# Kernel optimization log

Hardware: AMD Instinct MI355X
Metric: run time of the kernel (lower is better)

The kernel has to match this reference:

```python
import jax, jax.numpy as jnp
import numpy as np

B, C, H, W = 8, 256, 128, 128
P = 7          # patch_size (odd)
N = 500        # n_infer (eval mode)
HIDDEN = C // 16  # reduction=16


def setup_inputs() -> dict:
    key = jax.random.key(0)
    ks = jax.random.split(key, 8)
    def s(k, shape, fan_in):
        return jax.random.normal(k, shape, jnp.float32) * (1.0 / np.sqrt(fan_in))
    return {
        "x_main": jax.random.normal(ks[0], (B, C, H, W), jnp.float32),
        "x_aux": jax.random.normal(ks[1], (B, C, H, W), jnp.float32),
        "scorer_w": s(ks[2], (C,), C),            # 1x1 conv C->1
        "scorer_b": s(ks[3], (1,), C),
        "fc1_w": s(ks[4], (3 * C, HIDDEN), 3 * C),
        "fc1_b": jnp.zeros((HIDDEN,), jnp.float32),
        "fc2_w": s(ks[5], (HIDDEN, C), HIDDEN),
        "fc2_b": jnp.zeros((C,), jnp.float32),
        "proj_w": s(ks[6], (C, C), C),
        "proj_b": jnp.zeros((C,), jnp.float32),
        "n": N,
    }


def _sample_patch_feats(feat, px, py):
    # feat: [C,H,W]; px,py: [n,p,p] pixel coords (align_corners=False convention).
    # Bilinear sample with zero padding, then pool 0.5*(mean+max) over the patch.
    c, h, w = feat.shape
    x0 = jnp.floor(px); y0 = jnp.floor(py)
    wx1 = px - x0; wy1 = py - y0
    def gather(yi, xi):
        valid = ((yi >= 0) & (yi < h) & (xi >= 0) & (xi < w)).astype(feat.dtype)
        yc = jnp.clip(yi, 0, h - 1).astype(jnp.int32)
        xc = jnp.clip(xi, 0, w - 1).astype(jnp.int32)
        return feat[:, yc, xc] * valid  # [C,n,p,p]
    patch = (gather(y0, x0) * ((1 - wy1) * (1 - wx1))
             + gather(y0, x0 + 1) * ((1 - wy1) * wx1)
             + gather(y0 + 1, x0) * (wy1 * (1 - wx1))
             + gather(y0 + 1, x0 + 1) * (wy1 * wx1))  # [C,n,p,p]
    v = 0.5 * (patch.mean(axis=(2, 3)) + patch.max(axis=(2, 3)))  # [C,n]
    return v.T  # [n,C]


def reference(x_main, x_aux, scorer_w, scorer_b, fc1_w, fc1_b, fc2_w, fc2_b, proj_w, proj_b, n):
    b, c, h, w = x_main.shape
    # saliency scores -> topk indices over flattened HW
    score = jax.nn.sigmoid(jnp.einsum('bchw,c->bhw', x_main, scorer_w) + scorer_b[0])
    score = score.reshape(b, h * w)
    _, idx = jax.lax.top_k(score, n)  # [b,n] int32
    idx_y = idx // w
    idx_x = idx - idx_y * w
    # build the (clamped) normalized grid exactly as the torch module does,
    # then convert to pixel coords: px = ((g+1)*W - 1)/2 (align_corners=False)
    r = P // 2
    d = jnp.arange(-r, r + 1, dtype=jnp.float32)
    yy, xx = jnp.meshgrid(d, d, indexing='ij')
    off_x = xx * (2.0 / w); off_y = yy * (2.0 / h)           # [p,p]
    cx = (idx_x.astype(jnp.float32) + 0.5) * (2.0 / w) - 1.0  # [b,n]
    cy = (idx_y.astype(jnp.float32) + 0.5) * (2.0 / h) - 1.0
    gx = jnp.clip(cx[:, :, None, None] + off_x, -1.0, 1.0)    # [b,n,p,p]
    gy = jnp.clip(cy[:, :, None, None] + off_y, -1.0, 1.0)
    px = ((gx + 1.0) * w - 1.0) * 0.5
    py = ((gy + 1.0) * h - 1.0) * 0.5
    sample = jax.vmap(_sample_patch_feats)
    v_main = sample(x_main, px, py)  # [b,n,C]
    v_aux = sample(x_aux, px, py)    # aux_in_proj is Identity (c_main==c_aux)
    # instance-level cross attention
    sim = jnp.einsum('bnc,bmc->bnm', v_main, v_aux) / jnp.sqrt(jnp.float32(c))
    attn = jax.nn.softmax(sim, axis=-1)
    v_hat = jnp.einsum('bnm,bmc->bnc', attn, v_aux)
    # gated fusion MLP
    z = jnp.concatenate([v_main, v_hat, v_main - v_hat], axis=-1)  # [b,n,3C]
    gate = jax.nn.sigmoid(jax.nn.relu(z @ fc1_w + fc1_b) @ fc2_w + fc2_b)
    v_fused = v_main + gate * (v_main - v_hat)
    v_inj = v_fused @ proj_w + proj_b  # [b,n,C]
    # scatter-add reinjection at the topk locations
    inject = jnp.zeros((b, h * w, c), x_main.dtype)
    inject = inject.at[jnp.arange(b)[:, None], idx].add(v_inj)
    inject = inject.reshape(b, h, w, c).transpose(0, 3, 1, 2)
    return x_main + inject
```

## Files before the change

### kernel.cpp

```cpp
#include <hip/hip_runtime.h>
#include <cstdint>
#include <cstddef>

#define HW    16384
#define CCH   256
#define WID   128
#define NB    8
#define NSEL  500
#define NPAD  512
#define CPG   16

__device__ __forceinline__ unsigned key_of(float f) {
  unsigned u = __float_as_uint(f);
  return (u & 0x80000000u) ? ~u : (u | 0x80000000u);
}

__global__ __launch_bounds__(256) void score_kernel(const float* __restrict__ x,
                                                    const float* __restrict__ w,
                                                    float* __restrict__ logits) {
  __shared__ float ws[CCH];
  int tid = threadIdx.x;
  ws[tid] = w[tid];
  __syncthreads();
  int pix = blockIdx.x * 256 + tid;
  int b = pix >> 14, p = pix & (HW - 1);
  const float* xp = x + ((size_t)b << 22) + p;
  float acc = 0.f;
#pragma unroll 16
  for (int c = 0; c < CCH; c++) acc += xp[(size_t)c * HW] * ws[c];
  logits[pix] = acc;
}

__global__ __launch_bounds__(1024) void topk_kernel(const float* __restrict__ logits,
                                                    int* __restrict__ idx_out,
                                                    int* __restrict__ map) {
  int b = blockIdx.x, tid = threadIdx.x;
  int lane = tid & 63, wave = tid >> 6;
  const float* lg = logits + (size_t)b * HW;
  __shared__ unsigned hist[256];
  __shared__ unsigned wtot[4];
  __shared__ unsigned wsum[16];
  __shared__ unsigned bc_prefix;
  __shared__ int bc_want;
  __shared__ int cnt;

  unsigned kreg[16];
#pragma unroll
  for (int j = 0; j < 4; j++) {
    float4 v = *(const float4*)&lg[tid * 16 + j * 4];
    kreg[4 * j + 0] = key_of(v.x);
    kreg[4 * j + 1] = key_of(v.y);
    kreg[4 * j + 2] = key_of(v.z);
    kreg[4 * j + 3] = key_of(v.w);
  }
  for (int p = tid; p < HW; p += 1024) map[(size_t)b * HW + p] = -1;

  unsigned prefix = 0;
  int want = NSEL;
  for (int shift = 24; shift >= 0; shift -= 8) {
    if (tid < 256) hist[tid] = 0;
    __syncthreads();
#pragma unroll
    for (int j = 0; j < 16; j++) {
      unsigned u = kreg[j];
      bool m = (shift == 24) || ((u >> (shift + 8)) == (prefix >> (shift + 8)));
      if (m) atomicAdd(&hist[(u >> shift) & 255u], 1u);
    }
    __syncthreads();
    unsigned h = (tid < 256) ? hist[tid] : 0u;
    unsigned v = h;
#pragma unroll
    for (int o = 1; o < 64; o <<= 1) {
      unsigned t = __shfl_down(v, o);
      if (lane < 64 - o) v += t;
    }
    if (tid < 256 && lane == 0) wtot[wave] = v;
    __syncthreads();
    if (tid < 256) {
      unsigned sfx = v;
      for (int w2 = wave + 1; w2 < 4; w2++) sfx += wtot[w2];
      unsigned above = sfx - h;
      if ((int)sfx >= want && (int)above < want) {
        bc_prefix = prefix | ((unsigned)tid << shift);
        bc_want = want - (int)above;
      }
    }
    __syncthreads();
    prefix = bc_prefix;
    want = bc_want;
  }
  unsigned thr = prefix;

  int local = 0;
#pragma unroll
  for (int j = 0; j < 16; j++) local += (kreg[j] == thr) ? 1 : 0;
  unsigned pv = (unsigned)local;
#pragma unroll
  for (int o = 1; o < 64; o <<= 1) {
    unsigned t = __shfl_up(pv, o);
    if (lane >= o) pv += t;
  }
  if (lane == 63) wsum[wave] = pv;
  if (tid == 0) cnt = 0;
  __syncthreads();
  unsigned woff = 0;
  for (int w2 = 0; w2 < wave; w2++) woff += wsum[w2];
  int rank = (int)(woff + pv) - local;
#pragma unroll
  for (int j = 0; j < 16; j++) {
    unsigned u = kreg[j];
    bool take = (u > thr);
    if (u == thr) { if (rank < want) take = true; rank++; }
    if (take) {
      int s = atomicAdd(&cnt, 1);
      int p = tid * 16 + j;
      idx_out[b * NPAD + s] = p;
      map[(size_t)b * HW + p] = s;
    }
  }
}

__device__ __forceinline__ void patch_weights(int p, int* xc, int* yc, float* wx, float* wy) {
  int iy = p >> 7, ix = p & (WID - 1);
#pragma unroll
  for (int d = 0; d < 7; d++) {
    int t = ix + d - 3;
    bool in = (t >= 0) && (t < WID);
    xc[d] = in ? t : (t < 0 ? 0 : WID - 1);
    wx[d] = in ? 1.f : 0.5f;
    t = iy + d - 3;
    in = (t >= 0) && (t < WID);
    yc[d] = in ? t : (t < 0 ? 0 : WID - 1);
    wy[d] = in ? 1.f : 0.5f;
  }
}

__global__ __launch_bounds__(512) void gather_dma_kernel(const float* __restrict__ xm,
                                                         const float* __restrict__ xa,
                                                         const int* __restrict__ idx,
                                                         float* __restrict__ vmainT,
                                                         float* __restrict__ vauxT) {
  extern __shared__ float plane2[];
  int g = blockIdx.x, b = blockIdx.y, z = blockIdx.z;
  int tid = threadIdx.x;
  int c0 = g * CPG;
  const float* src = (z == 0 ? xm : xa) + ((size_t)(b * CCH + c0)) * HW;
  float* dst = (z == 0 ? vmainT : vauxT) + (((size_t)(b * CCH + c0)) << 9);

  int t500 = (tid < NSEL) ? tid : 0;
  int p = idx[b * NPAD + t500];
  float wx[7], wy[7];
  int xc[7], yc[7], rb[7];
  patch_weights(p, xc, yc, wx, wy);
#pragma unroll
  for (int d = 0; d < 7; d++) rb[d] = yc[d] * WID;

#pragma unroll
  for (int j = 0; j < 8; j++) {
    int off = (tid + j * 512) * 4;
    __builtin_amdgcn_global_load_lds(
        (const __attribute__((address_space(1))) float*)(src + off),
        (__attribute__((address_space(3))) float*)(plane2 + off), 16, 0, 0);
  }
  __syncthreads();

  for (int c = 0; c < CPG; c++) {
    float* cur = plane2 + ((c & 1) ? HW : 0);
    float* nxt = plane2 + ((c & 1) ? 0 : HW);
    if (c + 1 < CPG) {
      const float* s2 = src + (size_t)(c + 1) * HW;
#pragma unroll
      for (int j = 0; j < 8; j++) {
        int off = (tid + j * 512) * 4;
        __builtin_amdgcn_global_load_lds(
            (const __attribute__((address_space(1))) float*)(s2 + off),
            (__attribute__((address_space(3))) float*)(nxt + off), 16, 0, 0);
      }
    }
    if (tid < NSEL) {
      float s = 0.f, mx = -INFINITY;
#pragma unroll
      for (int dy = 0; dy < 7; dy++) {
        float rs = 0.f, rm = -INFINITY;
        int rbb = rb[dy];
        float wyd = wy[dy];
#pragma unroll
        for (int dx = 0; dx < 7; dx++) {
          float v = cur[rbb + xc[dx]] * wx[dx];
          rs += v;
          rm = fmaxf(rm, v);
        }
        s += rs * wyd;
        mx = fmaxf(mx, rm * wyd);
      }
      dst[((size_t)c << 9) + tid] = 0.5f * (s * (1.f / 49.f) + mx);
    } else {
      dst[((size_t)c << 9) + tid] = 0.f;
    }
    __syncthreads();
  }
}

template <int M, int N, int K, bool AT, bool BT, bool BSHARED, int EPI>
__global__ __launch_bounds__(256) void gemm_kernel(const float* __restrict__ A,
                                                   const float* __restrict__ B,
                                                   float* __restrict__ C,
                                                   const float* __restrict__ bias) {
  constexpr int BM = 64, BN = 64, BK = 16;
  __shared__ float As[BK][BM + 4];
  __shared__ float Bs[BK][BN + 4];
  int tid = threadIdx.x;
  int bx = blockIdx.x, by = blockIdx.y, b = blockIdx.z;
  const float* Ab = A + (size_t)b * M * K;
  const float* Bb = BSHARED ? B : (B + (size_t)b * ((size_t)K * N));
  int tx = tid & 15, ty = tid >> 4;
  float acc[4][4] = {};

  for (int k0 = 0; k0 < K; k0 += BK) {
    if (!AT) {
      int ar = tid >> 2, ac4 = (tid & 3) * 4;
      const float4 av = *(const float4*)&Ab[(size_t)(by * BM + ar) * K + k0 + ac4];
      As[ac4 + 0][ar] = av.x; As[ac4 + 1][ar] = av.y;
      As[ac4 + 2][ar] = av.z; As[ac4 + 3][ar] = av.w;
    } else {
      int kr = tid >> 4, mc = (tid & 15) * 4;
      *(float4*)&As[kr][mc] = *(const float4*)&Ab[(size_t)(k0 + kr) * M + by * BM + mc];
    }
    if (!BT) {
      int br = tid >> 4, bc4 = (tid & 15) * 4;
      *(float4*)&Bs[br][bc4] = *(const float4*)&Bb[(size_t)(k0 + br) * N + bx * BN + bc4];
    } else {
      int nr = tid >> 2, kc4 = (tid & 3) * 4;
      const float4 bv = *(const float4*)&Bb[(size_t)(bx * BN + nr) * K + k0 + kc4];
      Bs[kc4 + 0][nr] = bv.x; Bs[kc4 + 1][nr] = bv.y;
      Bs[kc4 + 2][nr] = bv.z; Bs[kc4 + 3][nr] = bv.w;
    }
    __syncthreads();
#pragma unroll
    for (int kk = 0; kk < BK; kk++) {
      const float4 a = *(const float4*)&As[kk][ty * 4];
      const float4 bb = *(const float4*)&Bs[kk][tx * 4];
      float av[4] = {a.x, a.y, a.z, a.w};
      float bv[4] = {bb.x, bb.y, bb.z, bb.w};
#pragma unroll
      for (int rr = 0; rr < 4; rr++)
#pragma unroll
        for (int ss = 0; ss < 4; ss++) acc[rr][ss] += av[rr] * bv[ss];
    }
    __syncthreads();
  }
  if (EPI == 2) {
#pragma unroll
    for (int s = 0; s < 4; s++) {
      int col = bx * BN + tx * 4 + s;
      float bv = bias[col];
#pragma unroll
      for (int r = 0; r < 4; r++) {
        int row = by * BM + ty * 4 + r;
        C[((size_t)b * N + col) * M + row] = acc[r][s] + bv;
      }
    }
  } else {
    float scale = (EPI == 1) ? 0.0625f : 1.f;
#pragma unroll
    for (int r = 0; r < 4; r++) {
      int row = by * BM + ty * 4 + r;
#pragma unroll
      for (int s = 0; s < 4; s++) {
        int col = bx * BN + tx * 4 + s;
        C[((size_t)b * M + row) * N + col] = acc[r][s] * scale;
      }
    }
  }
}

__global__ __launch_bounds__(256) void softmax_kernel(float* __restrict__ sim) {
  int i = blockIdx.x, b = blockIdx.y, tid = threadIdx.x;
  float* row = sim + ((size_t)b * NPAD + i) * NPAD;
  float v0 = (tid < NSEL) ? row[tid] : -INFINITY;
  int j1 = tid + 256;
  float v1 = (j1 < NSEL) ? row[j1] : -INFINITY;
  float m = fmaxf(v0, v1);
  for (int o = 32; o; o >>= 1) m = fmaxf(m, __shfl_down(m, o));
  __shared__ float red[4];
  __shared__ float bm, bs;
  int wave = tid >> 6, lane = tid & 63;
  if (lane == 0) red[wave] = m;
  __syncthreads();
  if (tid == 0) bm = fmaxf(fmaxf(red[0], red[1]), fmaxf(red[2], red[3]));
  __syncthreads();
  m = bm;
  float e0 = (tid < NSEL) ? expf(v0 - m) : 0.f;
  float e1 = (j1 < NSEL) ? expf(v1 - m) : 0.f;
  float s = e0 + e1;
  for (int o = 32; o; o >>= 1) s += __shfl_down(s, o);
  if (lane == 0) red[wave] = s;
  __syncthreads();
  if (tid == 0) bs = 1.f / (red[0] + red[1] + red[2] + red[3]);
  __syncthreads();
  row[tid] = e0 * bs;
  row[j1] = e1 * bs;
}

__global__ __launch_bounds__(256) void mlp_kernel(const float* __restrict__ vmainT,
                                                  const float* __restrict__ vhat,
                                                  const float* __restrict__ fc1w,
                                                  const float* __restrict__ fc1b,
                                                  const float* __restrict__ fc2w,
                                                  const float* __restrict__ fc2b,
                                                  float* __restrict__ vfused) {
  int i = blockIdx.x, b = blockIdx.y, c = threadIdx.x;
  size_t base = ((size_t)b * NPAD + i) * CCH + c;
  float vm = vmainT[(((size_t)(b * CCH + c)) << 9) + i];
  float vh = vhat[base], vd = vm - vh;
  const float* w0 = fc1w + (size_t)c * 16;
  const float* w1 = fc1w + (size_t)(256 + c) * 16;
  const float* w2 = fc1w + (size_t)(512 + c) * 16;
  __shared__ float ph[256][17];
  __shared__ float part2[16][17];
  __shared__ float hsh[16];
#pragma unroll
  for (int k = 0; k < 16; k++) ph[c][k] = vm * w0[k] + vh * w1[k] + vd * w2[k];
  __syncthreads();
  int kk = c & 15, g = c >> 4;
  float part = 0.f;
#pragma unroll
  for (int j = 0; j < 16; j++) part += ph[g * 16 + j][kk];
  part2[g][kk] = part;
  __syncthreads();
  if (c < 16) {
    float s = fc1b[c];
#pragma unroll
    for (int g2 = 0; g2 < 16; g2++) s += part2[g2][c];
    hsh[c] = fmaxf(s, 0.f);
  }
  __syncthreads();
  float gte = fc2b[c];
#pragma unroll
  for (int k = 0; k < 16; k++) gte += hsh[k] * fc2w[k * 256 + c];
  gte = 1.f / (1.f + expf(-gte));
  vfused[base] = vm + gte * vd;
}

__global__ __launch_bounds__(256) void final_kernel(const float* __restrict__ x,
                                                    const int* __restrict__ map,
                                                    const float* __restrict__ vinjT,
                                                    float* __restrict__ out) {
  int gid = blockIdx.x * 256 + threadIdx.x;
  int p4 = gid & 4095;
  int c = (gid >> 12) & 255;
  int b = gid >> 20;
  size_t xoff = (((size_t)(b * 256 + c)) << 14) + ((size_t)p4 << 2);
  float4 xv = *(const float4*)(x + xoff);
  const int4 mv = *(const int4*)(map + ((size_t)b << 14) + (p4 << 2));
  const float* vt = vinjT + ((size_t)(b * 256 + c) << 9);
  if (mv.x >= 0) xv.x += vt[mv.x];
  if (mv.y >= 0) xv.y += vt[mv.y];
  if (mv.z >= 0) xv.z += vt[mv.z];
  if (mv.w >= 0) xv.w += vt[mv.w];
  *(float4*)(out + xoff) = xv;
}

extern "C" void kernel_launch(void* const* d_in, const int* in_sizes, int n_in,
                              void* d_out, int out_size, void* d_ws, size_t ws_size,
                              hipStream_t stream) {
  const float* x_main   = (const float*)d_in[0];
  const float* x_aux    = (const float*)d_in[1];
  const float* scorer_w = (const float*)d_in[2];
  const float* fc1_w = (const float*)d_in[4];
  const float* fc1_b = (const float*)d_in[5];
  const float* fc2_w = (const float*)d_in[6];
  const float* fc2_b = (const float*)d_in[7];
  const float* proj_w = (const float*)d_in[8];
  const float* proj_b = (const float*)d_in[9];
  (void)in_sizes; (void)n_in; (void)out_size; (void)ws_size;

  float* ws = (float*)d_ws;
  float* logits = ws;
  int*   idx    = (int*)(ws + 131072);
  int*   map    = (int*)(ws + 135168);
  float* vmainT = ws + 266240;
  float* vauxT  = ws + 1314816;
  float* vhat   = ws + 2363392;
  float* vfused = ws + 3411968;
  float* sim    = ws + 4460544;
  float* vinjT  = vhat;
  float* out = (float*)d_out;

  score_kernel<<<512, 256, 0, stream>>>(x_main, scorer_w, logits);
  topk_kernel<<<NB, 1024, 0, stream>>>(logits, idx, map);
  gather_dma_kernel<<<dim3(CCH / CPG, NB, 2), 512, 2 * HW * sizeof(float), stream>>>(
      x_main, x_aux, idx, vmainT, vauxT);
  gemm_kernel<NPAD, NPAD, CCH, true, false, false, 1>
      <<<dim3(8, 8, NB), 256, 0, stream>>>(vmainT, vauxT, sim, nullptr);
  softmax_kernel<<<dim3(NPAD, NB), 256, 0, stream>>>(sim);
  gemm_kernel<NPAD, CCH, NPAD, false, true, false, 0>
      <<<dim3(4, 8, NB), 256, 0, stream>>>(sim, vauxT, vhat, nullptr);
  mlp_kernel<<<dim3(NPAD, NB), 256, 0, stream>>>(vmainT, vhat, fc1_w, fc1_b,
                                                 fc2_w, fc2_b, vfused);
  gemm_kernel<NPAD, CCH, CCH, false, false, true, 2>
      <<<dim3(4, 8, NB), 256, 0, stream>>>(vfused, proj_w, vinjT, proj_b);
  final_kernel<<<32768, 256, 0, stream>>>(x_main, map, vinjT, out);
}
```

Measured before the change: 488.7 us.

## Fuse output copy into score pass and replace final pass with sparse scatter

The score kernel now writes x_main to the output with nontemporal stores while it reads it for the saliency dot product. That removes the final full-tensor read-and-write pass and the dense index map (its initialisation and lookups). Reinjection becomes a small scatter kernel that adds the projected vectors only at the top-k positions. The cost is an extra 128MB write inside the score kernel, which is a single pass with low parallelism (512 blocks), plus scattered read-modify-writes to the output.

```diff
diff --git a/kernel.cpp b/kernel.cpp
--- a/kernel.cpp
+++ b/kernel.cpp
@@ -15,9 +15,10 @@
   return (u & 0x80000000u) ? ~u : (u | 0x80000000u);
 }
 
-__global__ __launch_bounds__(256) void score_kernel(const float* __restrict__ x,
-                                                    const float* __restrict__ w,
-                                                    float* __restrict__ logits) {
+__global__ __launch_bounds__(256) void score_copy_kernel(const float* __restrict__ x,
+                                                         const float* __restrict__ w,
+                                                         float* __restrict__ logits,
+                                                         float* __restrict__ out) {
   __shared__ float ws[CCH];
   int tid = threadIdx.x;
   ws[tid] = w[tid];
@@ -25,15 +26,19 @@
   int pix = blockIdx.x * 256 + tid;
   int b = pix >> 14, p = pix & (HW - 1);
   const float* xp = x + ((size_t)b << 22) + p;
+  float* op = out + ((size_t)b << 22) + p;
   float acc = 0.f;
-#pragma unroll 16
-  for (int c = 0; c < CCH; c++) acc += xp[(size_t)c * HW] * ws[c];
+#pragma unroll 8
+  for (int c = 0; c < CCH; c++) {
+    float v = xp[(size_t)c * HW];
+    acc += v * ws[c];
+    __builtin_nontemporal_store(v, &op[(size_t)c * HW]);
+  }
   logits[pix] = acc;
 }
 
 __global__ __launch_bounds__(1024) void topk_kernel(const float* __restrict__ logits,
-                                                    int* __restrict__ idx_out,
-                                                    int* __restrict__ map) {
+                                                    int* __restrict__ idx_out) {
   int b = blockIdx.x, tid = threadIdx.x;
   int lane = tid & 63, wave = tid >> 6;
   const float* lg = logits + (size_t)b * HW;
@@ -53,7 +58,6 @@
     kreg[4 * j + 2] = key_of(v.z);
     kreg[4 * j + 3] = key_of(v.w);
   }
-  for (int p = tid; p < HW; p += 1024) map[(size_t)b * HW + p] = -1;
 
   unsigned prefix = 0;
   int want = NSEL;
@@ -113,9 +117,7 @@
     if (u == thr) { if (rank < want) take = true; rank++; }
     if (take) {
       int s = atomicAdd(&cnt, 1);
-      int p = tid * 16 + j;
-      idx_out[b * NPAD + s] = p;
-      map[(size_t)b * HW + p] = s;
+      idx_out[b * NPAD + s] = tid * 16 + j;
     }
   }
 }
@@ -342,23 +344,16 @@
   vfused[base] = vm + gte * vd;
 }
 
-__global__ __launch_bounds__(256) void final_kernel(const float* __restrict__ x,
-                                                    const int* __restrict__ map,
-                                                    const float* __restrict__ vinjT,
-                                                    float* __restrict__ out) {
-  int gid = blockIdx.x * 256 + threadIdx.x;
-  int p4 = gid & 4095;
-  int c = (gid >> 12) & 255;
-  int b = gid >> 20;
-  size_t xoff = (((size_t)(b * 256 + c)) << 14) + ((size_t)p4 << 2);
-  float4 xv = *(const float4*)(x + xoff);
-  const int4 mv = *(const int4*)(map + ((size_t)b << 14) + (p4 << 2));
-  const float* vt = vinjT + ((size_t)(b * 256 + c) << 9);
-  if (mv.x >= 0) xv.x += vt[mv.x];
-  if (mv.y >= 0) xv.y += vt[mv.y];
-  if (mv.z >= 0) xv.z += vt[mv.z];
-  if (mv.w >= 0) xv.w += vt[mv.w];
-  *(float4*)(out + xoff) = xv;
+__global__ __launch_bounds__(256) void scatter_kernel(const int* __restrict__ idx,
+                                                      const float* __restrict__ vinjT,
+                                                      float* __restrict__ out) {
+  int c = blockIdx.x, b = blockIdx.y, t = threadIdx.x;
+  float* op = out + ((size_t)(b * CCH + c) << 14);
+  const float* vp = vinjT + ((size_t)(b * CCH + c) << 9);
+  const int* ib = idx + b * NPAD;
+  op[ib[t]] += vp[t];
+  int s = t + 256;
+  if (s < NSEL) op[ib[s]] += vp[s];
 }
 
 extern "C" void kernel_launch(void* const* d_in, const int* in_sizes, int n_in,
@@ -378,7 +373,6 @@
   float* ws = (float*)d_ws;
   float* logits = ws;
   int*   idx    = (int*)(ws + 131072);
-  int*   map    = (int*)(ws + 135168);
   float* vmainT = ws + 266240;
   float* vauxT  = ws + 1314816;
   float* vhat   = ws + 2363392;
@@ -387,8 +381,8 @@
   float* vinjT  = vhat;
   float* out = (float*)d_out;
 
-  score_kernel<<<512, 256, 0, stream>>>(x_main, scorer_w, logits);
-  topk_kernel<<<NB, 1024, 0, stream>>>(logits, idx, map);
+  score_copy_kernel<<<512, 256, 0, stream>>>(x_main, scorer_w, logits, out);
+  topk_kernel<<<NB, 1024, 0, stream>>>(logits, idx);
   gather_dma_kernel<<<dim3(CCH / CPG, NB, 2), 512, 2 * HW * sizeof(float), stream>>>(
       x_main, x_aux, idx, vmainT, vauxT);
   gemm_kernel<NPAD, NPAD, CCH, true, false, false, 1>
@@ -400,5 +394,5 @@
                                                  fc2_w, fc2_b, vfused);
   gemm_kernel<NPAD, CCH, CCH, false, false, true, 2>
       <<<dim3(4, 8, NB), 256, 0, stream>>>(vfused, proj_w, vinjT, proj_b);
-  final_kernel<<<32768, 256, 0, stream>>>(x_main, map, vinjT, out);
-}
+  scatter_kernel<<<dim3(CCH, NB), 256, 0, stream>>>(idx, vinjT, out);
+}
```

Result: no change. 490.9 us (+0.5%).
